# Performance work log

Hardware: AMD Instinct MI355X
Metric: run time of the kernel (lower is better)

The kernel has to match this reference:

```python
import jax, jax.numpy as jnp
import numpy as np

# --- constants from init_kwargs / module defaults ---
H, W, C = 720, 1280, 2
T_EVT, T_PROP = 10, 10
T_TOTAL = T_EVT + T_PROP          # 20 temporal steps (10 event + 10 propagation)
TAU, THR0 = 10.0, 1.0             # LIF time constant, base threshold
ALPHA, TARGET_RATE = 0.1, 0.1     # PENT adaptation
THR_MIN, THR_MAX = 0.1, 10.0
N_EVENTS = 4_000_000


def setup_inputs() -> dict:
    key = jax.random.key(0)
    k1, k2, k3, k4 = jax.random.split(key, 4)
    x = jax.random.randint(k1, (N_EVENTS,), 0, W, dtype=jnp.int32)
    y = jax.random.randint(k2, (N_EVENTS,), 0, H, dtype=jnp.int32)
    p = jax.random.randint(k3, (N_EVENTS,), 0, 2, dtype=jnp.int32)
    t = jax.random.uniform(k4, (N_EVENTS,), dtype=jnp.float32)
    return {"x": x, "y": y, "p": p, "t": t}


def _build_buffer(x, y, p, t):
    # TemporalBuffer.forward: bin events into first T_EVT steps, rest are zeros.
    tmin, tmax = t.min(), t.max()
    denom = jnp.where(tmax > tmin, tmax - tmin, jnp.float32(1.0))
    t_norm = jnp.where(tmax > tmin, (t - tmin) / denom * (T_EVT - 1e-6), 0.0)
    t_idx = jnp.clip(t_norm.astype(jnp.int32), 0, T_EVT - 1)
    xi = jnp.clip(x, 0, W - 1)
    yi = jnp.clip(y, 0, H - 1)
    c_idx = p  # p in {0,1} -> channel index directly (p.min() >= 0 branch)
    buf = jnp.zeros((T_TOTAL, C, H, W), jnp.float32)
    return buf.at[t_idx, c_idx, yi, xi].add(1.0)


def reference(x, y, p, t):
    buffer = _build_buffer(x, y, p, t)  # (T, C, H, W)
    decay = jnp.float32(np.exp(-1.0 / TAU))

    def step(carry, frame):
        mem, thr = carry
        # LIFBuffer: decay + accumulate
        mem = mem * decay + frame
        spk = (mem >= thr).astype(jnp.float32)
        mem = mem - spk * thr  # soft ('subtract') reset
        # AdaptiveThreshold (PENT): homeostatic rate-based adaptation
        rate = spk.mean()
        thr = jnp.clip(thr + ALPHA * (rate - TARGET_RATE), THR_MIN, THR_MAX)
        return (mem, thr), spk

    mem0 = jnp.zeros((C, H, W), jnp.float32)
    (_, _), spikes = jax.lax.scan(step, (mem0, jnp.float32(THR0)), buffer)
    return spikes  # (T, C, H, W) binary spike activity maps
```

## Files before the change

### kernel.cpp

```cpp
#include <hip/hip_runtime.h>
#include <cstddef>

#define HH 720
#define WW 1280
#define FRAME 1843200
#define FRAME4 460800
#define T_EVT 10
#define T_TOTAL 20
#define ARRIVE64 (1ULL << 32)

#define ONBLK 256
#define ONTHR 1024
#define ONWPB 16
#define ONT (ONBLK * ONTHR)

#define SBLK 1024
#define STHR 256
#define SWPB 4
#define PIXB 1800
#define NGROUP4 450
#define HIST_W 9000
#define RBLK 512
#define RTHR 1024
#define OTHR 512
#define NBUCKET 1024

#define MAT_OFF   0u
#define CS_OFF    (512u * 1024u * 4u)
#define SB_OFF    (CS_OFF + 4096u)
#define KEY_OFF   (SB_OFF + 8192u)
#define SEG_OFF(n) (KEY_OFF + 4u * (unsigned)(n))
#define WS_NEED(n) ((size_t)SEG_OFF(n) + 2ull * (size_t)(n) + 256ull)

__device__ unsigned g_minkey;
__device__ unsigned g_maxkey;
__device__ unsigned g_part_mn[RBLK];
__device__ unsigned g_part_mx[RBLK];
__device__ unsigned long long g_grp[T_TOTAL][16][16];
__device__ unsigned long long g_top[T_TOTAL][16];
__device__ unsigned g_rel[T_TOTAL][32];
__device__ unsigned long long g_n1[T_TOTAL][64][16];
__device__ unsigned long long g_n2[T_TOTAL][4][16];
__device__ unsigned long long g_n3[T_TOTAL][16];
__device__ unsigned g_relg[T_TOTAL][64][32];

__device__ __forceinline__ unsigned f2key(float f) {
    unsigned b = __float_as_uint(f);
    return b ^ ((unsigned)(((int)b) >> 31) | 0x80000000u);
}
__device__ __forceinline__ float key2f(unsigned k) {
    unsigned b = (k & 0x80000000u) ? (k ^ 0x80000000u) : ~k;
    return __uint_as_float(b);
}

__device__ __forceinline__ int event_bin_t(float tv, float tmin, float tmax) {
#pragma clang fp contract(off)
    float tn;
    if (tmax > tmin) tn = (tv - tmin) / (tmax - tmin) * (float)(10.0 - 1e-6);
    else tn = 0.0f;
    int ti = (int)tn;
    return ti < 0 ? 0 : (ti > T_EVT - 1 ? T_EVT - 1 : ti);
}
__device__ __forceinline__ int event_pixel(int xi, int yi, int ci) {
    xi = xi < 0 ? 0 : (xi > WW - 1 ? WW - 1 : xi);
    yi = yi < 0 ? 0 : (yi > HH - 1 ? HH - 1 : yi);
    return ci * (HH * WW) + yi * WW + xi;
}

__global__ void init_kernel() {
    const int gtid = blockIdx.x * blockDim.x + threadIdx.x;
    const int gs = gridDim.x * blockDim.x;
    if (gtid == 0) { g_minkey = 0xFFFFFFFFu; g_maxkey = 0u; }
    unsigned long long* a = &g_grp[0][0][0];
    for (int i = gtid; i < T_TOTAL * 16 * 16; i += gs) a[i] = 0ull;
    unsigned long long* b = &g_top[0][0];
    for (int i = gtid; i < T_TOTAL * 16; i += gs) b[i] = 0ull;
    unsigned* c = &g_rel[0][0];
    for (int i = gtid; i < T_TOTAL * 32; i += gs) c[i] = 0u;
}

__device__ __forceinline__ void minmax_body(const float* __restrict__ t, int n,
                                            int gtid, int gstride) {
    unsigned mn = 0xFFFFFFFFu, mx = 0u;
    const int n4 = n >> 2;
    const float4* t4 = (const float4*)t;
    for (int i = gtid; i < n4; i += gstride) {
        float4 tv = t4[i];
        unsigned k0 = f2key(tv.x), k1 = f2key(tv.y);
        unsigned k2 = f2key(tv.z), k3 = f2key(tv.w);
        unsigned a = k0 < k1 ? k0 : k1, b = k2 < k3 ? k2 : k3;
        unsigned c = a < b ? a : b;
        mn = mn < c ? mn : c;
        a = k0 > k1 ? k0 : k1; b = k2 > k3 ? k2 : k3;
        c = a > b ? a : b;
        mx = mx > c ? mx : c;
    }
    for (int i = (n4 << 2) + gtid; i < n; i += gstride) {
        unsigned k = f2key(t[i]);
        mn = mn < k ? mn : k;
        mx = mx > k ? mx : k;
    }
    for (int off = 32; off > 0; off >>= 1) {
        unsigned omn = (unsigned)__shfl_down((int)mn, off, 64);
        unsigned omx = (unsigned)__shfl_down((int)mx, off, 64);
        mn = mn < omn ? mn : omn;
        mx = mx > omx ? mx : omx;
    }
    __shared__ unsigned smn[16], smx[16];
    int lane = threadIdx.x & 63, wv = threadIdx.x >> 6;
    if (lane == 0) { smn[wv] = mn; smx[wv] = mx; }
    __syncthreads();
    if (threadIdx.x == 0) {
        int nw = blockDim.x >> 6;
        for (int i = 1; i < nw; ++i) {
            mn = mn < smn[i] ? mn : smn[i];
            mx = mx > smx[i] ? mx : smx[i];
        }
        atomicMin(&g_minkey, mn);
        atomicMax(&g_maxkey, mx);
    }
}

__device__ __forceinline__ void minmax_part_body(const float* __restrict__ t, int n,
                                                 int gtid, int gstride) {
    unsigned mn = 0xFFFFFFFFu, mx = 0u;
    const int n4 = n >> 2;
    const float4* t4 = (const float4*)t;
    for (int i = gtid; i < n4; i += gstride) {
        float4 tv = t4[i];
        unsigned k0 = f2key(tv.x), k1 = f2key(tv.y);
        unsigned k2 = f2key(tv.z), k3 = f2key(tv.w);
        unsigned a = k0 < k1 ? k0 : k1, b = k2 < k3 ? k2 : k3;
        unsigned c = a < b ? a : b;
        mn = mn < c ? mn : c;
        a = k0 > k1 ? k0 : k1; b = k2 > k3 ? k2 : k3;
        c = a > b ? a : b;
        mx = mx > c ? mx : c;
    }
    for (int i = (n4 << 2) + gtid; i < n; i += gstride) {
        unsigned k = f2key(t[i]);
        mn = mn < k ? mn : k;
        mx = mx > k ? mx : k;
    }
    for (int off = 32; off > 0; off >>= 1) {
        unsigned omn = (unsigned)__shfl_down((int)mn, off, 64);
        unsigned omx = (unsigned)__shfl_down((int)mx, off, 64);
        mn = mn < omn ? mn : omn;
        mx = mx > omx ? mx : omx;
    }
    __shared__ unsigned smn[16], smx[16];
    int lane = threadIdx.x & 63, wv = threadIdx.x >> 6;
    if (lane == 0) { smn[wv] = mn; smx[wv] = mx; }
    __syncthreads();
    if (threadIdx.x == 0) {
        int nw = blockDim.x >> 6;
        for (int i = 1; i < nw; ++i) {
            mn = mn < smn[i] ? mn : smn[i];
            mx = mx > smx[i] ? mx : smx[i];
        }
        g_part_mn[blockIdx.x] = mn;
        g_part_mx[blockIdx.x] = mx;
    }
}

__global__ void minmax_zero_kernel(const float* __restrict__ t, int n,
                                   uint4* __restrict__ hist16v) {
    const int gtid = blockIdx.x * blockDim.x + threadIdx.x;
    const int gstride = gridDim.x * blockDim.x;
    const uint4 z = make_uint4(0u, 0u, 0u, 0u);
    const int nz = T_EVT * FRAME / 8;
    for (int i = gtid; i < nz; i += gstride) hist16v[i] = z;
    minmax_body(t, n, gtid, gstride);
}

__global__ __launch_bounds__(RTHR) void passA_kernel(
        const int* __restrict__ x, const int* __restrict__ y,
        const int* __restrict__ p, const float* __restrict__ t,
        unsigned* __restrict__ mat, unsigned* __restrict__ keys, int n) {
    __shared__ unsigned cnt[NBUCKET];
    const int gtid = blockIdx.x * blockDim.x + threadIdx.x;
    const int gs = gridDim.x * blockDim.x;
    {
        unsigned long long* z1 = &g_n1[0][0][0];
        for (int i = gtid; i < T_TOTAL * 64 * 16; i += gs) z1[i] = 0ull;
        unsigned long long* z2 = &g_n2[0][0][0];
        for (int i = gtid; i < T_TOTAL * 4 * 16; i += gs) z2[i] = 0ull;
        unsigned long long* z3 = &g_n3[0][0];
        for (int i = gtid; i < T_TOTAL * 16; i += gs) z3[i] = 0ull;
        unsigned* z4 = &g_relg[0][0][0];
        for (int i = gtid; i < T_TOTAL * 64 * 32; i += gs) z4[i] = 0u;
    }
    for (int i = threadIdx.x; i < NBUCKET; i += blockDim.x) cnt[i] = 0u;
    __syncthreads();
    const int chunk = (n + (int)gridDim.x - 1) / (int)gridDim.x;
    const int s0 = blockIdx.x * chunk;
    const int s1 = min(n, s0 + chunk);
    for (int i = s0 + threadIdx.x; i < s1; i += blockDim.x) {
        int pix = event_pixel(x[i], y[i], p[i]);
        keys[i] = (unsigned)pix;
        atomicAdd(&cnt[pix / PIXB], 1u);
    }
    minmax_part_body(t, n, gtid, gs);
    __syncthreads();
    for (int i = threadIdx.x; i < NBUCKET; i += blockDim.x)
        mat[blockIdx.x * NBUCKET + i] = cnt[i];
}

__global__ __launch_bounds__(OTHR) void offsets_col_kernel(
        unsigned* __restrict__ mat, unsigned* __restrict__ colsum) {
    const int j = blockIdx.x;
    const int r = threadIdx.x;
    const int lane = r & 63, wv = r >> 6;
    unsigned v = mat[r * NBUCKET + j];
    unsigned incl = v;
    for (int off = 1; off < 64; off <<= 1) {
        unsigned o = (unsigned)__shfl_up((int)incl, off, 64);
        if (lane >= off) incl += o;
    }
    __shared__ unsigned wtot[OTHR / 64];
    if (lane == 63) wtot[wv] = incl;
    __syncthreads();
    if (r == 0) {
        unsigned run = 0;
#pragma unroll
        for (int k = 0; k < OTHR / 64; ++k) { unsigned tmp = wtot[k]; wtot[k] = run; run += tmp; }
    }
    __syncthreads();
    unsigned ex = incl - v + wtot[wv];
    mat[r * NBUCKET + j] = ex;
    if (r == OTHR - 1) colsum[j] = ex + v;

    if (j == 0) {
        unsigned mn = g_part_mn[r], mx = g_part_mx[r];
        for (int off = 32; off > 0; off >>= 1) {
            unsigned omn = (unsigned)__shfl_down((int)mn, off, 64);
            unsigned omx = (unsigned)__shfl_down((int)mx, off, 64);
            mn = mn < omn ? mn : omn;
            mx = mx > omx ? mx : omx;
        }
        __shared__ unsigned smn2[OTHR / 64], smx2[OTHR / 64];
        if (lane == 0) { smn2[wv] = mn; smx2[wv] = mx; }
        __syncthreads();
        if (r == 0) {
#pragma unroll
            for (int k = 1; k < OTHR / 64; ++k) {
                mn = mn < smn2[k] ? mn : smn2[k];
                mx = mx > smx2[k] ? mx : smx2[k];
            }
            g_minkey = mn;
            g_maxkey = mx;
        }
    }
}

__global__ __launch_bounds__(RTHR) void passB_kernel(
        const unsigned* __restrict__ keys, const float* __restrict__ t,
        const unsigned* __restrict__ mat, const unsigned* __restrict__ colsum,
        unsigned* __restrict__ seg_base_out,
        unsigned short* __restrict__ seg, int n) {
    __shared__ unsigned base[NBUCKET];
    __shared__ unsigned wt2[RTHR / 64];
    {
        const int j = threadIdx.x;
        const int lane = j & 63, wv = j >> 6;
        unsigned v = colsum[j];
        unsigned incl = v;
        for (int off = 1; off < 64; off <<= 1) {
            unsigned o = (unsigned)__shfl_up((int)incl, off, 64);
            if (lane >= off) incl += o;
        }
        if (lane == 63) wt2[wv] = incl;
        __syncthreads();
        if (j == 0) {
            unsigned run = 0;
#pragma unroll
            for (int k = 0; k < RTHR / 64; ++k) { unsigned tmp = wt2[k]; wt2[k] = run; run += tmp; }
        }
        __syncthreads();
        unsigned ex = incl - v + wt2[wv];
        base[j] = mat[blockIdx.x * NBUCKET + j] + ex;
        if (blockIdx.x == 0) {
            seg_base_out[j] = ex;
            if (j == NBUCKET - 1) seg_base_out[NBUCKET] = ex + v;
        }
    }
    __syncthreads();
    const float tmin = key2f(g_minkey);
    const float tmax = key2f(g_maxkey);
    const int chunk = (n + (int)gridDim.x - 1) / (int)gridDim.x;
    const int s0 = blockIdx.x * chunk;
    const int s1 = min(n, s0 + chunk);
    for (int i = s0 + threadIdx.x; i < s1; i += blockDim.x) {
        int pix = (int)keys[i];
        int ti = event_bin_t(t[i], tmin, tmax);
        int bkt = pix / PIXB;
        int lb = ti * PIXB + (pix - bkt * PIXB);
        unsigned idx = atomicAdd(&base[bkt], 1u);
        seg[idx] = (unsigned short)lb;
    }
}

__global__ __launch_bounds__(STHR, 4) void scan_new(float* __restrict__ out,
                                                    const unsigned short* __restrict__ seg,
                                                    const unsigned* __restrict__ seg_base) {
#pragma clang fp contract(off)
    const float decay = (float)0.9048374180359595;
    const int tid = threadIdx.x;
    const int lane = tid & 63;
    const int b = blockIdx.x;
    const int pix0 = b * PIXB;

    __shared__ alignas(16) unsigned lds_hist[HIST_W];
    __shared__ unsigned lds_arr[T_TOTAL];
    __shared__ unsigned lds_tot[T_TOTAL];

    for (int i = tid; i < HIST_W; i += STHR) lds_hist[i] = 0u;
    if (tid < T_TOTAL) { lds_arr[tid] = 0u; lds_tot[tid] = 0u; }
    __syncthreads();

    {
        const int e0 = (int)seg_base[b];
        const int e1 = (int)seg_base[b + 1];
        for (int i = e0 + tid; i < e1; i += STHR) {
            unsigned lb = seg[i];
            atomicAdd(&lds_hist[lb >> 1], 1u << ((lb & 1u) << 4));
        }
    }
    __syncthreads();

    const bool has1 = tid < (NGROUP4 - STHR);
    float4 mem0 = make_float4(0.f, 0.f, 0.f, 0.f);
    float4 mem1 = make_float4(0.f, 0.f, 0.f, 0.f);
    float thr = 1.0f;

    float4 f0, f1;
    {
        uint2 w01 = *(const uint2*)&lds_hist[tid << 1];
        f0 = make_float4((float)(w01.x & 0xFFFFu), (float)(w01.x >> 16),
                         (float)(w01.y & 0xFFFFu), (float)(w01.y >> 16));
        if (has1) {
            uint2 v = *(const uint2*)&lds_hist[(tid + STHR) << 1];
            f1 = make_float4((float)(v.x & 0xFFFFu), (float)(v.x >> 16),
                             (float)(v.y & 0xFFFFu), (float)(v.y >> 16));
        } else f1 = make_float4(0.f, 0.f, 0.f, 0.f);
    }

    for (int s = 0;; ++s) {
        float* ob = out + (size_t)s * FRAME + pix0;
        int cnt = 0;

        {
            float4 m, spk;
            m.x = mem0.x + f0.x;
            m.y = mem0.y + f0.y;
            m.z = mem0.z + f0.z;
            m.w = mem0.w + f0.w;
            spk.x = (m.x >= thr) ? 1.0f : 0.0f;
            spk.y = (m.y >= thr) ? 1.0f : 0.0f;
            spk.z = (m.z >= thr) ? 1.0f : 0.0f;
            spk.w = (m.w >= thr) ? 1.0f : 0.0f;
            ((float4*)ob)[tid] = spk;
            mem0.x = m.x - spk.x * thr;
            mem0.y = m.y - spk.y * thr;
            mem0.z = m.z - spk.z * thr;
            mem0.w = m.w - spk.w * thr;
            cnt += (int)spk.x + (int)spk.y + (int)spk.z + (int)spk.w;
        }
        if (has1) {
            int g = tid + STHR;
            float4 m, spk;
            m.x = mem1.x + f1.x;
            m.y = mem1.y + f1.y;
            m.z = mem1.z + f1.z;
            m.w = mem1.w + f1.w;
            spk.x = (m.x >= thr) ? 1.0f : 0.0f;
            spk.y = (m.y >= thr) ? 1.0f : 0.0f;
            spk.z = (m.z >= thr) ? 1.0f : 0.0f;
            spk.w = (m.w >= thr) ? 1.0f : 0.0f;
            ((float4*)ob)[g] = spk;
            mem1.x = m.x - spk.x * thr;
            mem1.y = m.y - spk.y * thr;
            mem1.z = m.z - spk.z * thr;
            mem1.w = m.w - spk.w * thr;
            cnt += (int)spk.x + (int)spk.y + (int)spk.z + (int)spk.w;
        }

        if (s == T_TOTAL - 1) break;

        for (int off = 32; off > 0; off >>= 1) cnt += __shfl_down(cnt, off, 64);

        bool last = false;
        const int g1 = b >> 4;
        if (lane == 0) {
            unsigned old = __hip_atomic_fetch_add(&lds_arr[s],
                               (unsigned)cnt + (1u << 16),
                               __ATOMIC_RELAXED, __HIP_MEMORY_SCOPE_WORKGROUP);
            if ((old >> 16) == SWPB - 1) {
                last = true;
                unsigned bc = (old + (unsigned)cnt) & 0xFFFFu;
                unsigned long long a1 = __hip_atomic_fetch_add(
                    &g_n1[s][g1][0], (unsigned long long)bc + ARRIVE64,
                    __ATOMIC_RELAXED, __HIP_MEMORY_SCOPE_AGENT);
                if ((unsigned)(a1 >> 32) == 15u) {
                    unsigned c1 = (unsigned)a1 + bc;
                    const int g2 = g1 >> 4;
                    unsigned long long a2 = __hip_atomic_fetch_add(
                        &g_n2[s][g2][0], (unsigned long long)c1 + ARRIVE64,
                        __ATOMIC_RELAXED, __HIP_MEMORY_SCOPE_AGENT);
                    if ((unsigned)(a2 >> 32) == 15u) {
                        unsigned c2 = (unsigned)a2 + c1;
                        unsigned long long a3 = __hip_atomic_fetch_add(
                            &g_n3[s][0], (unsigned long long)c2 + ARRIVE64,
                            __ATOMIC_RELAXED, __HIP_MEMORY_SCOPE_AGENT);
                        if ((unsigned)(a3 >> 32) == 3u) {
                            unsigned tot = (unsigned)a3 + c2;
                            for (int g = 0; g < 64; ++g)
                                __hip_atomic_store(&g_relg[s][g][0], tot + 1u,
                                    __ATOMIC_RELAXED, __HIP_MEMORY_SCOPE_AGENT);
                        }
                    }
                }
            }
        }

        {
            const int sn = s + 1;
            if (sn < T_EVT) {
                uint2 w01 = *(const uint2*)&lds_hist[sn * 900 + (tid << 1)];
                f0 = make_float4((float)(w01.x & 0xFFFFu), (float)(w01.x >> 16),
                                 (float)(w01.y & 0xFFFFu), (float)(w01.y >> 16));
                if (has1) {
                    uint2 v = *(const uint2*)&lds_hist[sn * 900 + ((tid + STHR) << 1)];
                    f1 = make_float4((float)(v.x & 0xFFFFu), (float)(v.x >> 16),
                                     (float)(v.y & 0xFFFFu), (float)(v.y >> 16));
                }
            } else {
                f0 = make_float4(0.f, 0.f, 0.f, 0.f);
                f1 = make_float4(0.f, 0.f, 0.f, 0.f);
            }
            mem0.x = mem0.x * decay; mem0.y = mem0.y * decay;
            mem0.z = mem0.z * decay; mem0.w = mem0.w * decay;
            mem1.x = mem1.x * decay; mem1.y = mem1.y * decay;
            mem1.z = mem1.z * decay; mem1.w = mem1.w * decay;
        }
        __builtin_amdgcn_sched_barrier(0);

        unsigned total = 0u;
        if (lane == 0) {
            unsigned f;
            if (last) {
                do {
                    __builtin_amdgcn_s_sleep(1);
                    f = __hip_atomic_load(&g_relg[s][g1][0], __ATOMIC_RELAXED,
                                          __HIP_MEMORY_SCOPE_AGENT);
                } while (f == 0u);
                total = f - 1u;
                __hip_atomic_store(&lds_tot[s], f,
                                   __ATOMIC_RELAXED, __HIP_MEMORY_SCOPE_WORKGROUP);
            } else {
                unsigned f2;
                do {
                    __builtin_amdgcn_s_sleep(1);
                    f2 = __hip_atomic_load(&lds_tot[s], __ATOMIC_RELAXED,
                                           __HIP_MEMORY_SCOPE_WORKGROUP);
                } while (f2 == 0u);
                total = f2 - 1u;
            }
        }
        total = (unsigned)__shfl((int)total, 0, 64);
        float rate = (float)total / 1843200.0f;
        thr = thr + 0.1f * (rate - 0.1f);
        thr = fminf(fmaxf(thr, 0.1f), 10.0f);
    }
}

__global__ void scatter_kernel(const int* __restrict__ x, const int* __restrict__ y,
                               const int* __restrict__ p, const float* __restrict__ t,
                               unsigned* __restrict__ hist32, int n) {
    int i = blockIdx.x * blockDim.x + threadIdx.x;
    if (i >= n) return;
    float tmin = key2f(g_minkey);
    float tmax = key2f(g_maxkey);
    int ti = event_bin_t(t[i], tmin, tmax);
    int pix = event_pixel(x[i], y[i], p[i]);
    size_t bidx = (size_t)ti * FRAME + pix;
    atomicAdd(hist32 + (bidx >> 1), 1u << ((bidx & 1) << 4));
}

__global__ __launch_bounds__(ONTHR) void scan_old(float* __restrict__ out) {
#pragma clang fp contract(off)
    const float decay = (float)0.9048374180359595;
    const int gtid = blockIdx.x * ONTHR + threadIdx.x;
    const int lane = threadIdx.x & 63;
    const uint2 uz2 = make_uint2(0u, 0u);
    float4 mem0 = make_float4(0.f, 0.f, 0.f, 0.f);
    float4 mem1 = make_float4(0.f, 0.f, 0.f, 0.f);
    const bool has1 = (gtid + ONT) < FRAME4;
    float thr = 1.0f;
    const uint2* hist2 = (const uint2*)(out + (size_t)T_EVT * FRAME);
    __shared__ unsigned lds_arr[T_TOTAL];
    __shared__ unsigned lds_tot[T_TOTAL];
    if (threadIdx.x < T_TOTAL) { lds_arr[threadIdx.x] = 0u; lds_tot[threadIdx.x] = 0u; }
    __syncthreads();
    uint2 u0 = hist2[gtid];
    uint2 u1 = has1 ? hist2[gtid + ONT] : uz2;
    for (int s = 0; s < T_TOTAL; ++s) {
        float4* o4 = (float4*)(out + (size_t)s * FRAME);
        int cnt = 0;
        {
            float4 m, spk;
            m.x = mem0.x * decay; m.x = m.x + (float)(u0.x & 0xFFFFu);
            m.y = mem0.y * decay; m.y = m.y + (float)(u0.x >> 16);
            m.z = mem0.z * decay; m.z = m.z + (float)(u0.y & 0xFFFFu);
            m.w = mem0.w * decay; m.w = m.w + (float)(u0.y >> 16);
            spk.x = (m.x >= thr) ? 1.0f : 0.0f;
            spk.y = (m.y >= thr) ? 1.0f : 0.0f;
            spk.z = (m.z >= thr) ? 1.0f : 0.0f;
            spk.w = (m.w >= thr) ? 1.0f : 0.0f;
            o4[gtid] = spk;
            mem0.x = m.x - spk.x * thr; mem0.y = m.y - spk.y * thr;
            mem0.z = m.z - spk.z * thr; mem0.w = m.w - spk.w * thr;
            cnt += (int)spk.x + (int)spk.y + (int)spk.z + (int)spk.w;
        }
        if (has1) {
            float4 m, spk;
            m.x = mem1.x * decay; m.x = m.x + (float)(u1.x & 0xFFFFu);
            m.y = mem1.y * decay; m.y = m.y + (float)(u1.x >> 16);
            m.z = mem1.z * decay; m.z = m.z + (float)(u1.y & 0xFFFFu);
            m.w = mem1.w * decay; m.w = m.w + (float)(u1.y >> 16);
            spk.x = (m.x >= thr) ? 1.0f : 0.0f;
            spk.y = (m.y >= thr) ? 1.0f : 0.0f;
            spk.z = (m.z >= thr) ? 1.0f : 0.0f;
            spk.w = (m.w >= thr) ? 1.0f : 0.0f;
            o4[gtid + ONT] = spk;
            mem1.x = m.x - spk.x * thr; mem1.y = m.y - spk.y * thr;
            mem1.z = m.z - spk.z * thr; mem1.w = m.w - spk.w * thr;
            cnt += (int)spk.x + (int)spk.y + (int)spk.z + (int)spk.w;
        }
        if (s + 1 < T_EVT) {
            const uint2* hn = hist2 + (size_t)(s + 1) * FRAME4;
            u0 = hn[gtid];
            u1 = has1 ? hn[gtid + ONT] : uz2;
        } else { u0 = uz2; u1 = uz2; }
        if (s == T_TOTAL - 1) break;
        for (int off = 32; off > 0; off >>= 1) cnt += __shfl_down(cnt, off, 64);
        unsigned total = 0u;
        if (lane == 0) {
            unsigned old = __hip_atomic_fetch_add(&lds_arr[s],
                               (unsigned)cnt + (1u << 16),
                               __ATOMIC_RELAXED, __HIP_MEMORY_SCOPE_WORKGROUP);
            if ((old >> 16) == ONWPB - 1) {
                unsigned bc = (old + (unsigned)cnt) & 0xFFFFu;
                const int gid = blockIdx.x >> 4;
                unsigned long long gold = __hip_atomic_fetch_add(
                    &g_grp[s][gid][0], (unsigned long long)bc + ARRIVE64,
                    __ATOMIC_RELAXED, __HIP_MEMORY_SCOPE_AGENT);
                if ((unsigned)(gold >> 32) == 15u) {
                    unsigned gc = (unsigned)gold + bc;
                    unsigned long long told = __hip_atomic_fetch_add(
                        &g_top[s][0], (unsigned long long)gc + ARRIVE64,
                        __ATOMIC_RELAXED, __HIP_MEMORY_SCOPE_AGENT);
                    if ((unsigned)(told >> 32) == 15u) {
                        unsigned tot = (unsigned)told + gc;
                        __hip_atomic_store(&g_rel[s][0], tot + 1u,
                                           __ATOMIC_RELAXED, __HIP_MEMORY_SCOPE_AGENT);
                    }
                }
                unsigned f;
                do {
                    __builtin_amdgcn_s_sleep(1);
                    f = __hip_atomic_load(&g_rel[s][0], __ATOMIC_RELAXED,
                                          __HIP_MEMORY_SCOPE_AGENT);
                } while (f == 0u);
                total = f - 1u;
                __hip_atomic_store(&lds_tot[s], f,
                                   __ATOMIC_RELAXED, __HIP_MEMORY_SCOPE_WORKGROUP);
            } else {
                unsigned f;
                do {
                    __builtin_amdgcn_s_sleep(1);
                    f = __hip_atomic_load(&lds_tot[s], __ATOMIC_RELAXED,
                                          __HIP_MEMORY_SCOPE_WORKGROUP);
                } while (f == 0u);
                total = f - 1u;
            }
        }
        total = (unsigned)__shfl((int)total, 0, 64);
        float rate = (float)total / 1843200.0f;
        thr = thr + 0.1f * (rate - 0.1f);
        thr = fminf(fmaxf(thr, 0.1f), 10.0f);
    }
}

extern "C" void kernel_launch(void* const* d_in, const int* in_sizes, int n_in,
                              void* d_out, int out_size, void* d_ws, size_t ws_size,
                              hipStream_t stream) {
    const int*   x = (const int*)d_in[0];
    const int*   y = (const int*)d_in[1];
    const int*   p = (const int*)d_in[2];
    const float* t = (const float*)d_in[3];
    float* out = (float*)d_out;
    const int n = in_sizes[0];

    if (d_ws != nullptr && ws_size >= WS_NEED(n)) {
        unsigned* mat = (unsigned*)((char*)d_ws + MAT_OFF);
        unsigned* colsum = (unsigned*)((char*)d_ws + CS_OFF);
        unsigned* seg_base = (unsigned*)((char*)d_ws + SB_OFF);
        unsigned* keys = (unsigned*)((char*)d_ws + KEY_OFF);
        unsigned short* seg = (unsigned short*)((char*)d_ws + SEG_OFF(n));

        passA_kernel<<<RBLK, RTHR, 0, stream>>>(x, y, p, t, mat, keys, n);
        offsets_col_kernel<<<NBUCKET, OTHR, 0, stream>>>(mat, colsum);
        passB_kernel<<<RBLK, RTHR, 0, stream>>>(keys, t, mat, colsum, seg_base, seg, n);

        dim3 g(SBLK), b(STHR);
        void* args[] = { (void*)&out, (void*)&seg, (void*)&seg_base };
        hipLaunchCooperativeKernel((void*)scan_new, g, b, args, 0, stream);
    } else {
        init_kernel<<<64, 256, 0, stream>>>();
        unsigned* hist32 = (unsigned*)(out + (size_t)T_EVT * FRAME);
        minmax_zero_kernel<<<1024, 256, 0, stream>>>(t, n, (uint4*)hist32);
        scatter_kernel<<<(n + 255) / 256, 256, 0, stream>>>(x, y, p, t, hist32, n);
        dim3 g(ONBLK), b(ONTHR);
        void* args[] = { (void*)&out };
        hipLaunchCooperativeKernel((void*)scan_old, g, b, args, 0, stream);
    }
}
```

Baseline: 344.9 us.

## Locally sort events in LDS before bucket scatter and fuse min/max into passA

passB now runs half as many blocks, each covering two passA chunks. Each block counting-sorts its events by bucket in shared memory, then writes them out as contiguous runs per bucket, replacing random 2-byte global scatter writes. passA computes the timestamp min/max inside its main event loop instead of a separate grid-stride float4 pass over t. The cost is heavy LDS use (about 88KB per block), lower occupancy for passB, and a new size guard that falls back to the old path for large n.

```diff
diff --git a/kernel.cpp b/kernel.cpp
--- a/kernel.cpp
+++ b/kernel.cpp
@@ -24,6 +24,9 @@
 #define RTHR 1024
 #define OTHR 512
 #define NBUCKET 1024
+#define BBLK (RBLK / 2)
+#define EPT 20
+#define MAXM (EPT * RTHR)
 
 #define MAT_OFF   0u
 #define CS_OFF    (512u * 1024u * 4u)
@@ -118,48 +121,6 @@
         }
         atomicMin(&g_minkey, mn);
         atomicMax(&g_maxkey, mx);
-    }
-}
-
-__device__ __forceinline__ void minmax_part_body(const float* __restrict__ t, int n,
-                                                 int gtid, int gstride) {
-    unsigned mn = 0xFFFFFFFFu, mx = 0u;
-    const int n4 = n >> 2;
-    const float4* t4 = (const float4*)t;
-    for (int i = gtid; i < n4; i += gstride) {
-        float4 tv = t4[i];
-        unsigned k0 = f2key(tv.x), k1 = f2key(tv.y);
-        unsigned k2 = f2key(tv.z), k3 = f2key(tv.w);
-        unsigned a = k0 < k1 ? k0 : k1, b = k2 < k3 ? k2 : k3;
-        unsigned c = a < b ? a : b;
-        mn = mn < c ? mn : c;
-        a = k0 > k1 ? k0 : k1; b = k2 > k3 ? k2 : k3;
-        c = a > b ? a : b;
-        mx = mx > c ? mx : c;
-    }
-    for (int i = (n4 << 2) + gtid; i < n; i += gstride) {
-        unsigned k = f2key(t[i]);
-        mn = mn < k ? mn : k;
-        mx = mx > k ? mx : k;
-    }
-    for (int off = 32; off > 0; off >>= 1) {
-        unsigned omn = (unsigned)__shfl_down((int)mn, off, 64);
-        unsigned omx = (unsigned)__shfl_down((int)mx, off, 64);
-        mn = mn < omn ? mn : omn;
-        mx = mx > omx ? mx : omx;
-    }
-    __shared__ unsigned smn[16], smx[16];
-    int lane = threadIdx.x & 63, wv = threadIdx.x >> 6;
-    if (lane == 0) { smn[wv] = mn; smx[wv] = mx; }
-    __syncthreads();
-    if (threadIdx.x == 0) {
-        int nw = blockDim.x >> 6;
-        for (int i = 1; i < nw; ++i) {
-            mn = mn < smn[i] ? mn : smn[i];
-            mx = mx > smx[i] ? mx : smx[i];
-        }
-        g_part_mn[blockIdx.x] = mn;
-        g_part_mx[blockIdx.x] = mx;
     }
 }
 
@@ -192,16 +153,37 @@
     }
     for (int i = threadIdx.x; i < NBUCKET; i += blockDim.x) cnt[i] = 0u;
     __syncthreads();
-    const int chunk = (n + (int)gridDim.x - 1) / (int)gridDim.x;
+    const int chunk = (n + RBLK - 1) / RBLK;
     const int s0 = blockIdx.x * chunk;
     const int s1 = min(n, s0 + chunk);
+    unsigned mn = 0xFFFFFFFFu, mx = 0u;
     for (int i = s0 + threadIdx.x; i < s1; i += blockDim.x) {
         int pix = event_pixel(x[i], y[i], p[i]);
         keys[i] = (unsigned)pix;
         atomicAdd(&cnt[pix / PIXB], 1u);
-    }
-    minmax_part_body(t, n, gtid, gs);
-    __syncthreads();
+        unsigned k = f2key(t[i]);
+        mn = mn < k ? mn : k;
+        mx = mx > k ? mx : k;
+    }
+    for (int off = 32; off > 0; off >>= 1) {
+        unsigned omn = (unsigned)__shfl_down((int)mn, off, 64);
+        unsigned omx = (unsigned)__shfl_down((int)mx, off, 64);
+        mn = mn < omn ? mn : omn;
+        mx = mx > omx ? mx : omx;
+    }
+    __shared__ unsigned smn[RTHR / 64], smx[RTHR / 64];
+    const int lane = threadIdx.x & 63, wv = threadIdx.x >> 6;
+    if (lane == 0) { smn[wv] = mn; smx[wv] = mx; }
+    __syncthreads();
+    if (threadIdx.x == 0) {
+#pragma unroll
+        for (int i = 1; i < RTHR / 64; ++i) {
+            mn = mn < smn[i] ? mn : smn[i];
+            mx = mx > smx[i] ? mx : smx[i];
+        }
+        g_part_mn[blockIdx.x] = mn;
+        g_part_mx[blockIdx.x] = mx;
+    }
     for (int i = threadIdx.x; i < NBUCKET; i += blockDim.x)
         mat[blockIdx.x * NBUCKET + i] = cnt[i];
 }
@@ -259,10 +241,13 @@
         unsigned* __restrict__ seg_base_out,
         unsigned short* __restrict__ seg, int n) {
     __shared__ unsigned base[NBUCKET];
+    __shared__ unsigned lrun[NBUCKET];
     __shared__ unsigned wt2[RTHR / 64];
+    __shared__ unsigned short sorted[MAXM];
+    __shared__ unsigned short sbkt[MAXM];
+    const int j = threadIdx.x;
+    const int lane = j & 63, wv = j >> 6;
     {
-        const int j = threadIdx.x;
-        const int lane = j & 63, wv = j >> 6;
         unsigned v = colsum[j];
         unsigned incl = v;
         for (int off = 1; off < 64; off <<= 1) {
@@ -278,7 +263,8 @@
         }
         __syncthreads();
         unsigned ex = incl - v + wt2[wv];
-        base[j] = mat[blockIdx.x * NBUCKET + j] + ex;
+        base[j] = mat[(2 * blockIdx.x) * NBUCKET + j] + ex;
+        lrun[j] = 0u;
         if (blockIdx.x == 0) {
             seg_base_out[j] = ex;
             if (j == NBUCKET - 1) seg_base_out[NBUCKET] = ex + v;
@@ -287,16 +273,60 @@
     __syncthreads();
     const float tmin = key2f(g_minkey);
     const float tmax = key2f(g_maxkey);
-    const int chunk = (n + (int)gridDim.x - 1) / (int)gridDim.x;
-    const int s0 = blockIdx.x * chunk;
-    const int s1 = min(n, s0 + chunk);
-    for (int i = s0 + threadIdx.x; i < s1; i += blockDim.x) {
-        int pix = (int)keys[i];
-        int ti = event_bin_t(t[i], tmin, tmax);
-        int bkt = pix / PIXB;
-        int lb = ti * PIXB + (pix - bkt * PIXB);
-        unsigned idx = atomicAdd(&base[bkt], 1u);
-        seg[idx] = (unsigned short)lb;
+    const int cA = (n + RBLK - 1) / RBLK;
+    const int s0 = blockIdx.x * 2 * cA;
+    const int s1 = min(n, s0 + 2 * cA);
+    const int m = s1 - s0;
+
+    unsigned rec[EPT];
+#pragma unroll
+    for (int k = 0; k < EPT; ++k) {
+        rec[k] = 0xFFFFFFFFu;
+        int i = s0 + k * RTHR + j;
+        if (i < s1) {
+            int pix = (int)keys[i];
+            int ti = event_bin_t(t[i], tmin, tmax);
+            int bkt = pix / PIXB;
+            int lb = ti * PIXB + (pix - bkt * PIXB);
+            rec[k] = ((unsigned)bkt << 16) | (unsigned)lb;
+            atomicAdd(&lrun[bkt], 1u);
+        }
+    }
+    __syncthreads();
+    {
+        unsigned v = lrun[j];
+        unsigned incl = v;
+        for (int off = 1; off < 64; off <<= 1) {
+            unsigned o = (unsigned)__shfl_up((int)incl, off, 64);
+            if (lane >= off) incl += o;
+        }
+        if (lane == 63) wt2[wv] = incl;
+        __syncthreads();
+        if (j == 0) {
+            unsigned run = 0;
+#pragma unroll
+            for (int k = 0; k < RTHR / 64; ++k) { unsigned tmp = wt2[k]; wt2[k] = run; run += tmp; }
+        }
+        __syncthreads();
+        unsigned ex = incl - v + wt2[wv];
+        base[j] -= ex;
+        lrun[j] = ex;
+    }
+    __syncthreads();
+#pragma unroll
+    for (int k = 0; k < EPT; ++k) {
+        unsigned r0 = rec[k];
+        if (r0 != 0xFFFFFFFFu) {
+            unsigned bkt = r0 >> 16;
+            unsigned r = atomicAdd(&lrun[bkt], 1u);
+            sorted[r] = (unsigned short)(r0 & 0xFFFFu);
+            sbkt[r] = (unsigned short)bkt;
+        }
+    }
+    __syncthreads();
+    for (int i = j; i < m; i += RTHR) {
+        unsigned bk = sbkt[i];
+        seg[base[bk] + (unsigned)i] = sorted[i];
     }
 }
 
@@ -602,7 +632,8 @@
     float* out = (float*)d_out;
     const int n = in_sizes[0];
 
-    if (d_ws != nullptr && ws_size >= WS_NEED(n)) {
+    const int cA = (n + RBLK - 1) / RBLK;
+    if (d_ws != nullptr && ws_size >= WS_NEED(n) && 2 * cA <= MAXM) {
         unsigned* mat = (unsigned*)((char*)d_ws + MAT_OFF);
         unsigned* colsum = (unsigned*)((char*)d_ws + CS_OFF);
         unsigned* seg_base = (unsigned*)((char*)d_ws + SB_OFF);
@@ -611,7 +642,7 @@
 
         passA_kernel<<<RBLK, RTHR, 0, stream>>>(x, y, p, t, mat, keys, n);
         offsets_col_kernel<<<NBUCKET, OTHR, 0, stream>>>(mat, colsum);
-        passB_kernel<<<RBLK, RTHR, 0, stream>>>(keys, t, mat, colsum, seg_base, seg, n);
+        passB_kernel<<<BBLK, RTHR, 0, stream>>>(keys, t, mat, colsum, seg_base, seg, n);
 
         dim3 g(SBLK), b(STHR);
         void* args[] = { (void*)&out, (void*)&seg, (void*)&seg_base };
```

After: 321.7 us. 6.7% less time.

## Fuse event binning passes with per-block local sort and separate minmax kernel

Applied to the files above, without the earlier changes.

Replaces the three-kernel count/offset/scatter pipeline with a separate minmax kernel followed by one fused pass. Each block bins its chunk of events, sorts them locally in shared memory by bucket, and writes them contiguously along with packed per-bucket offset and count words. The scan kernel then gathers each bucket's events from the 512 per-block runs, so no global column prefix scan or global atomic scatter is needed. The costs are an extra memset and kernel launch, a larger shared-memory footprint in the fused pass, and a scan-side gather made of many short, serialized per-run loops.

```diff
diff --git a/kernel.cpp b/kernel.cpp
--- a/kernel.cpp
+++ b/kernel.cpp
@@ -22,20 +22,19 @@
 #define HIST_W 9000
 #define RBLK 512
 #define RTHR 1024
-#define OTHR 512
 #define NBUCKET 1024
+#define EPT 8
+#define MAXM (EPT * RTHR)
+#define MMBLK 128
+#define MMTHR 1024
 
 #define MAT_OFF   0u
-#define CS_OFF    (512u * 1024u * 4u)
-#define SB_OFF    (CS_OFF + 4096u)
-#define KEY_OFF   (SB_OFF + 8192u)
-#define SEG_OFF(n) (KEY_OFF + 4u * (unsigned)(n))
-#define WS_NEED(n) ((size_t)SEG_OFF(n) + 2ull * (size_t)(n) + 256ull)
+#define MMX_OFF   (512u * 1024u * 4u)
+#define KEY_OFF   (MMX_OFF + 4096u)
+#define WS_NEED(chunk) ((size_t)KEY_OFF + 2ull * RBLK * (size_t)(chunk) + 256ull)
 
 __device__ unsigned g_minkey;
 __device__ unsigned g_maxkey;
-__device__ unsigned g_part_mn[RBLK];
-__device__ unsigned g_part_mx[RBLK];
 __device__ unsigned long long g_grp[T_TOTAL][16][16];
 __device__ unsigned long long g_top[T_TOTAL][16];
 __device__ unsigned g_rel[T_TOTAL][32];
@@ -121,48 +120,6 @@
     }
 }
 
-__device__ __forceinline__ void minmax_part_body(const float* __restrict__ t, int n,
-                                                 int gtid, int gstride) {
-    unsigned mn = 0xFFFFFFFFu, mx = 0u;
-    const int n4 = n >> 2;
-    const float4* t4 = (const float4*)t;
-    for (int i = gtid; i < n4; i += gstride) {
-        float4 tv = t4[i];
-        unsigned k0 = f2key(tv.x), k1 = f2key(tv.y);
-        unsigned k2 = f2key(tv.z), k3 = f2key(tv.w);
-        unsigned a = k0 < k1 ? k0 : k1, b = k2 < k3 ? k2 : k3;
-        unsigned c = a < b ? a : b;
-        mn = mn < c ? mn : c;
-        a = k0 > k1 ? k0 : k1; b = k2 > k3 ? k2 : k3;
-        c = a > b ? a : b;
-        mx = mx > c ? mx : c;
-    }
-    for (int i = (n4 << 2) + gtid; i < n; i += gstride) {
-        unsigned k = f2key(t[i]);
-        mn = mn < k ? mn : k;
-        mx = mx > k ? mx : k;
-    }
-    for (int off = 32; off > 0; off >>= 1) {
-        unsigned omn = (unsigned)__shfl_down((int)mn, off, 64);
-        unsigned omx = (unsigned)__shfl_down((int)mx, off, 64);
-        mn = mn < omn ? mn : omn;
-        mx = mx > omx ? mx : omx;
-    }
-    __shared__ unsigned smn[16], smx[16];
-    int lane = threadIdx.x & 63, wv = threadIdx.x >> 6;
-    if (lane == 0) { smn[wv] = mn; smx[wv] = mx; }
-    __syncthreads();
-    if (threadIdx.x == 0) {
-        int nw = blockDim.x >> 6;
-        for (int i = 1; i < nw; ++i) {
-            mn = mn < smn[i] ? mn : smn[i];
-            mx = mx > smx[i] ? mx : smx[i];
-        }
-        g_part_mn[blockIdx.x] = mn;
-        g_part_mx[blockIdx.x] = mx;
-    }
-}
-
 __global__ void minmax_zero_kernel(const float* __restrict__ t, int n,
                                    uint4* __restrict__ hist16v) {
     const int gtid = blockIdx.x * blockDim.x + threadIdx.x;
@@ -173,13 +130,65 @@
     minmax_body(t, n, gtid, gstride);
 }
 
-__global__ __launch_bounds__(RTHR) void passA_kernel(
+__global__ __launch_bounds__(MMTHR) void minmax_ws_kernel(
+        const float* __restrict__ t, int n, unsigned* __restrict__ mmx) {
+    const int gtid = blockIdx.x * blockDim.x + threadIdx.x;
+    const int gstride = gridDim.x * blockDim.x;
+    unsigned mx = 0u, imn = 0u;
+    const int n4 = n >> 2;
+    const float4* t4 = (const float4*)t;
+    for (int i = gtid; i < n4; i += gstride) {
+        float4 tv = t4[i];
+        unsigned k0 = f2key(tv.x), k1 = f2key(tv.y);
+        unsigned k2 = f2key(tv.z), k3 = f2key(tv.w);
+        unsigned a = k0 > k1 ? k0 : k1, b = k2 > k3 ? k2 : k3;
+        unsigned c = a > b ? a : b;
+        mx = mx > c ? mx : c;
+        unsigned i0 = ~k0, i1 = ~k1, i2 = ~k2, i3 = ~k3;
+        a = i0 > i1 ? i0 : i1; b = i2 > i3 ? i2 : i3;
+        c = a > b ? a : b;
+        imn = imn > c ? imn : c;
+    }
+    for (int i = (n4 << 2) + gtid; i < n; i += gstride) {
+        unsigned k = f2key(t[i]);
+        mx = mx > k ? mx : k;
+        unsigned ik = ~k;
+        imn = imn > ik ? imn : ik;
+    }
+    for (int off = 32; off > 0; off >>= 1) {
+        unsigned omx = (unsigned)__shfl_down((int)mx, off, 64);
+        unsigned oim = (unsigned)__shfl_down((int)imn, off, 64);
+        mx = mx > omx ? mx : omx;
+        imn = imn > oim ? imn : oim;
+    }
+    __shared__ unsigned smx[MMTHR / 64], sim[MMTHR / 64];
+    const int lane = threadIdx.x & 63, wv = threadIdx.x >> 6;
+    if (lane == 0) { smx[wv] = mx; sim[wv] = imn; }
+    __syncthreads();
+    if (threadIdx.x == 0) {
+#pragma unroll
+        for (int i = 1; i < MMTHR / 64; ++i) {
+            mx = mx > smx[i] ? mx : smx[i];
+            imn = imn > sim[i] ? imn : sim[i];
+        }
+        atomicMax(&mmx[0], mx);
+        atomicMax(&mmx[32], imn);
+    }
+}
+
+__global__ __launch_bounds__(RTHR) void passAB_kernel(
         const int* __restrict__ x, const int* __restrict__ y,
         const int* __restrict__ p, const float* __restrict__ t,
-        unsigned* __restrict__ mat, unsigned* __restrict__ keys, int n) {
+        const unsigned* __restrict__ mmx,
+        unsigned* __restrict__ mat, unsigned short* __restrict__ seg, int n) {
     __shared__ unsigned cnt[NBUCKET];
-    const int gtid = blockIdx.x * blockDim.x + threadIdx.x;
-    const int gs = gridDim.x * blockDim.x;
+    __shared__ unsigned wt2[RTHR / 64];
+    __shared__ unsigned short sorted[MAXM];
+    const int bid = blockIdx.x;
+    const int j = threadIdx.x;
+    const int lane = j & 63, wv = j >> 6;
+    const int gtid = bid * RTHR + j;
+    const int gs = RBLK * RTHR;
     {
         unsigned long long* z1 = &g_n1[0][0][0];
         for (int i = gtid; i < T_TOTAL * 64 * 16; i += gs) z1[i] = 0ull;
@@ -190,80 +199,57 @@
         unsigned* z4 = &g_relg[0][0][0];
         for (int i = gtid; i < T_TOTAL * 64 * 32; i += gs) z4[i] = 0u;
     }
-    for (int i = threadIdx.x; i < NBUCKET; i += blockDim.x) cnt[i] = 0u;
-    __syncthreads();
-    const int chunk = (n + (int)gridDim.x - 1) / (int)gridDim.x;
-    const int s0 = blockIdx.x * chunk;
+    cnt[j] = 0u;
+    __syncthreads();
+    const float tmax = key2f(mmx[0]);
+    const float tmin = key2f(~mmx[32]);
+    const int chunk = (((n + RBLK - 1) / RBLK) + 3) & ~3;
+    const int s0 = bid * chunk;
     const int s1 = min(n, s0 + chunk);
-    for (int i = s0 + threadIdx.x; i < s1; i += blockDim.x) {
-        int pix = event_pixel(x[i], y[i], p[i]);
-        keys[i] = (unsigned)pix;
-        atomicAdd(&cnt[pix / PIXB], 1u);
-    }
-    minmax_part_body(t, n, gtid, gs);
-    __syncthreads();
-    for (int i = threadIdx.x; i < NBUCKET; i += blockDim.x)
-        mat[blockIdx.x * NBUCKET + i] = cnt[i];
-}
-
-__global__ __launch_bounds__(OTHR) void offsets_col_kernel(
-        unsigned* __restrict__ mat, unsigned* __restrict__ colsum) {
-    const int j = blockIdx.x;
-    const int r = threadIdx.x;
-    const int lane = r & 63, wv = r >> 6;
-    unsigned v = mat[r * NBUCKET + j];
-    unsigned incl = v;
-    for (int off = 1; off < 64; off <<= 1) {
-        unsigned o = (unsigned)__shfl_up((int)incl, off, 64);
-        if (lane >= off) incl += o;
-    }
-    __shared__ unsigned wtot[OTHR / 64];
-    if (lane == 63) wtot[wv] = incl;
-    __syncthreads();
-    if (r == 0) {
-        unsigned run = 0;
+    const int m = s1 - s0;
+
+    unsigned rec[EPT];
 #pragma unroll
-        for (int k = 0; k < OTHR / 64; ++k) { unsigned tmp = wtot[k]; wtot[k] = run; run += tmp; }
-    }
-    __syncthreads();
-    unsigned ex = incl - v + wtot[wv];
-    mat[r * NBUCKET + j] = ex;
-    if (r == OTHR - 1) colsum[j] = ex + v;
-
-    if (j == 0) {
-        unsigned mn = g_part_mn[r], mx = g_part_mx[r];
-        for (int off = 32; off > 0; off >>= 1) {
-            unsigned omn = (unsigned)__shfl_down((int)mn, off, 64);
-            unsigned omx = (unsigned)__shfl_down((int)mx, off, 64);
-            mn = mn < omn ? mn : omn;
-            mx = mx > omx ? mx : omx;
-        }
-        __shared__ unsigned smn2[OTHR / 64], smx2[OTHR / 64];
-        if (lane == 0) { smn2[wv] = mn; smx2[wv] = mx; }
-        __syncthreads();
-        if (r == 0) {
+    for (int k = 0; k < EPT / 4; ++k) {
+        const int ibase = s0 + ((k * RTHR + j) << 2);
 #pragma unroll
-            for (int k = 1; k < OTHR / 64; ++k) {
-                mn = mn < smn2[k] ? mn : smn2[k];
-                mx = mx > smx2[k] ? mx : smx2[k];
+        for (int e = 0; e < 4; ++e) rec[k * 4 + e] = 0xFFFFFFFFu;
+        if (ibase + 4 <= s1) {
+            int4 xv = *(const int4*)(x + ibase);
+            int4 yv = *(const int4*)(y + ibase);
+            int4 pv = *(const int4*)(p + ibase);
+            float4 tv = *(const float4*)(t + ibase);
+            int pxs[4] = { event_pixel(xv.x, yv.x, pv.x),
+                           event_pixel(xv.y, yv.y, pv.y),
+                           event_pixel(xv.z, yv.z, pv.z),
+                           event_pixel(xv.w, yv.w, pv.w) };
+            float ts[4] = { tv.x, tv.y, tv.z, tv.w };
+#pragma unroll
+            for (int e = 0; e < 4; ++e) {
+                int pix = pxs[e];
+                int ti = event_bin_t(ts[e], tmin, tmax);
+                int bkt = pix / PIXB;
+                int lb = ti * PIXB + (pix - bkt * PIXB);
+                rec[k * 4 + e] = ((unsigned)bkt << 16) | (unsigned)lb;
+                atomicAdd(&cnt[bkt], 1u);
             }
-            g_minkey = mn;
-            g_maxkey = mx;
-        }
-    }
-}
-
-__global__ __launch_bounds__(RTHR) void passB_kernel(
-        const unsigned* __restrict__ keys, const float* __restrict__ t,
-        const unsigned* __restrict__ mat, const unsigned* __restrict__ colsum,
-        unsigned* __restrict__ seg_base_out,
-        unsigned short* __restrict__ seg, int n) {
-    __shared__ unsigned base[NBUCKET];
-    __shared__ unsigned wt2[RTHR / 64];
+        } else if (ibase < s1) {
+            for (int e = 0; e < 4; ++e) {
+                int i = ibase + e;
+                if (i < s1) {
+                    int pix = event_pixel(x[i], y[i], p[i]);
+                    int ti = event_bin_t(t[i], tmin, tmax);
+                    int bkt = pix / PIXB;
+                    int lb = ti * PIXB + (pix - bkt * PIXB);
+                    rec[k * 4 + e] = ((unsigned)bkt << 16) | (unsigned)lb;
+                    atomicAdd(&cnt[bkt], 1u);
+                }
+            }
+        }
+    }
+    __syncthreads();
     {
-        const int j = threadIdx.x;
-        const int lane = j & 63, wv = j >> 6;
-        unsigned v = colsum[j];
+        unsigned v = cnt[j];
         unsigned incl = v;
         for (int off = 1; off < 64; off <<= 1) {
             unsigned o = (unsigned)__shfl_up((int)incl, off, 64);
@@ -278,31 +264,28 @@
         }
         __syncthreads();
         unsigned ex = incl - v + wt2[wv];
-        base[j] = mat[blockIdx.x * NBUCKET + j] + ex;
-        if (blockIdx.x == 0) {
-            seg_base_out[j] = ex;
-            if (j == NBUCKET - 1) seg_base_out[NBUCKET] = ex + v;
-        }
-    }
-    __syncthreads();
-    const float tmin = key2f(g_minkey);
-    const float tmax = key2f(g_maxkey);
-    const int chunk = (n + (int)gridDim.x - 1) / (int)gridDim.x;
-    const int s0 = blockIdx.x * chunk;
-    const int s1 = min(n, s0 + chunk);
-    for (int i = s0 + threadIdx.x; i < s1; i += blockDim.x) {
-        int pix = (int)keys[i];
-        int ti = event_bin_t(t[i], tmin, tmax);
-        int bkt = pix / PIXB;
-        int lb = ti * PIXB + (pix - bkt * PIXB);
-        unsigned idx = atomicAdd(&base[bkt], 1u);
-        seg[idx] = (unsigned short)lb;
-    }
+        mat[bid * NBUCKET + j] = (ex << 16) | v;
+        cnt[j] = ex;
+    }
+    __syncthreads();
+#pragma unroll
+    for (int k = 0; k < EPT; ++k) {
+        unsigned r0 = rec[k];
+        if (r0 != 0xFFFFFFFFu) {
+            unsigned bkt = r0 >> 16;
+            unsigned r = atomicAdd(&cnt[bkt], 1u);
+            sorted[r] = (unsigned short)(r0 & 0xFFFFu);
+        }
+    }
+    __syncthreads();
+    unsigned short* segb = seg + (size_t)bid * (size_t)chunk;
+    for (int i = j; i < m; i += RTHR) segb[i] = sorted[i];
 }
 
 __global__ __launch_bounds__(STHR, 4) void scan_new(float* __restrict__ out,
                                                     const unsigned short* __restrict__ seg,
-                                                    const unsigned* __restrict__ seg_base) {
+                                                    const unsigned* __restrict__ mat,
+                                                    int n) {
 #pragma clang fp contract(off)
     const float decay = (float)0.9048374180359595;
     const int tid = threadIdx.x;
@@ -311,19 +294,25 @@
     const int pix0 = b * PIXB;
 
     __shared__ alignas(16) unsigned lds_hist[HIST_W];
+    __shared__ unsigned runw[RBLK];
     __shared__ unsigned lds_arr[T_TOTAL];
     __shared__ unsigned lds_tot[T_TOTAL];
 
     for (int i = tid; i < HIST_W; i += STHR) lds_hist[i] = 0u;
+    for (int r = tid; r < RBLK; r += STHR) runw[r] = mat[r * NBUCKET + b];
     if (tid < T_TOTAL) { lds_arr[tid] = 0u; lds_tot[tid] = 0u; }
     __syncthreads();
 
     {
-        const int e0 = (int)seg_base[b];
-        const int e1 = (int)seg_base[b + 1];
-        for (int i = e0 + tid; i < e1; i += STHR) {
-            unsigned lb = seg[i];
-            atomicAdd(&lds_hist[lb >> 1], 1u << ((lb & 1u) << 4));
+        const int chunk = (((n + RBLK - 1) / RBLK) + 3) & ~3;
+        for (int r = tid; r < RBLK; r += STHR) {
+            unsigned w = runw[r];
+            unsigned c = w & 0xFFFFu;
+            const unsigned short* sp = seg + (size_t)r * (size_t)chunk + (w >> 16);
+            for (unsigned k = 0; k < c; ++k) {
+                unsigned lb = sp[k];
+                atomicAdd(&lds_hist[lb >> 1], 1u << ((lb & 1u) << 4));
+            }
         }
     }
     __syncthreads();
@@ -602,19 +591,18 @@
     float* out = (float*)d_out;
     const int n = in_sizes[0];
 
-    if (d_ws != nullptr && ws_size >= WS_NEED(n)) {
+    const int chunk = (((n + RBLK - 1) / RBLK) + 3) & ~3;
+    if (d_ws != nullptr && ws_size >= WS_NEED(chunk) && chunk <= MAXM && n >= 4) {
         unsigned* mat = (unsigned*)((char*)d_ws + MAT_OFF);
-        unsigned* colsum = (unsigned*)((char*)d_ws + CS_OFF);
-        unsigned* seg_base = (unsigned*)((char*)d_ws + SB_OFF);
-        unsigned* keys = (unsigned*)((char*)d_ws + KEY_OFF);
-        unsigned short* seg = (unsigned short*)((char*)d_ws + SEG_OFF(n));
-
-        passA_kernel<<<RBLK, RTHR, 0, stream>>>(x, y, p, t, mat, keys, n);
-        offsets_col_kernel<<<NBUCKET, OTHR, 0, stream>>>(mat, colsum);
-        passB_kernel<<<RBLK, RTHR, 0, stream>>>(keys, t, mat, colsum, seg_base, seg, n);
+        unsigned* mmx = (unsigned*)((char*)d_ws + MMX_OFF);
+        unsigned short* seg = (unsigned short*)((char*)d_ws + KEY_OFF);
+
+        hipMemsetAsync(mmx, 0, 256, stream);
+        minmax_ws_kernel<<<MMBLK, MMTHR, 0, stream>>>(t, n, mmx);
+        passAB_kernel<<<RBLK, RTHR, 0, stream>>>(x, y, p, t, mmx, mat, seg, n);
 
         dim3 g(SBLK), b(STHR);
-        void* args[] = { (void*)&out, (void*)&seg, (void*)&seg_base };
+        void* args[] = { (void*)&out, (void*)&seg, (void*)&mat, (void*)&n };
         hipLaunchCooperativeKernel((void*)scan_new, g, b, args, 0, stream);
     } else {
         init_kernel<<<64, 256, 0, stream>>>();
```

After: 307.7 us. -10.8%, faster.
